# Performance work log

Measured on AMD Instinct MI355X. Metric: run time of the kernel, lower is better.

## Reference

```python
import jax, jax.numpy as jnp
import numpy as np

N = 100000      # num nodes
E = 1600000     # num edges
DIN, H, DOUT = 64, 128, 64
EPS = 1e-5


def setup_inputs() -> dict:
    key = jax.random.key(0)
    ks = jax.random.split(key, 16)
    def w(k, shape):
        fan_in = shape[0]
        return jax.random.normal(k, shape, dtype=jnp.float32) / np.sqrt(fan_in)
    return {
        "x": jax.random.normal(ks[0], (N, DIN), dtype=jnp.float32),
        "edge_index": jax.random.randint(ks[1], (2, E), 0, N, dtype=jnp.int32),
        "W1": w(ks[2], (DIN, H)),  "b1": jnp.zeros((H,), jnp.float32),
        "W2": w(ks[3], (H, H)),    "b2": jnp.zeros((H,), jnp.float32),
        "W3": w(ks[4], (H, DOUT)), "b3": jnp.zeros((DOUT,), jnp.float32),
        "g1": jnp.ones((H,), jnp.float32),  "be1": jnp.zeros((H,), jnp.float32),
        "g2": jnp.ones((H,), jnp.float32),  "be2": jnp.zeros((H,), jnp.float32),
        "Ws1": w(ks[5], (DIN, H)),  "bs1": jnp.zeros((H,), jnp.float32),
        "Ws2": w(ks[6], (H, DOUT)), "bs2": jnp.zeros((DOUT,), jnp.float32),
    }


def _layer_norm(h, g, b):
    m = jnp.mean(h, axis=-1, keepdims=True)
    v = jnp.mean(jnp.square(h - m), axis=-1, keepdims=True)
    return (h - m) * jax.lax.rsqrt(v + EPS) * g + b


def reference(x, edge_index, W1, b1, W2, b2, W3, b3, g1, be1, g2, be2, Ws1, bs1, Ws2, bs2):
    n = x.shape[0]
    # GCNConv: add self-loops, symmetric deg^{-1/2} normalization (PyG default)
    loop = jnp.arange(n, dtype=edge_index.dtype)
    src = jnp.concatenate([edge_index[0], loop])  # [E+N]
    dst = jnp.concatenate([edge_index[1], loop])
    deg = jax.ops.segment_sum(jnp.ones_like(dst, dtype=x.dtype), dst, num_segments=n)
    dinv = jax.lax.rsqrt(deg)  # deg >= 1 thanks to self-loops
    norm = (dinv[src] * dinv[dst])[:, None]  # [E+N, 1]

    def conv(h, W, b):
        hw = h @ W                                   # [n, dout]
        msg = hw[src] * norm                         # gather + scale
        return jax.ops.segment_sum(msg, dst, num_segments=n) + b

    # layer 1: conv -> LN -> relu -> +skip1(x)   (dropout is eval-mode identity)
    x1 = jax.nn.relu(_layer_norm(conv(x, W1, b1), g1, be1)) + (x @ Ws1 + bs1)
    # layer 2: conv -> LN -> relu -> +x1
    x2 = jax.nn.relu(_layer_norm(conv(x1, W2, b2), g2, be2)) + x1
    # layer 3: conv + skip2(x1)
    x3 = conv(x2, W3, b3) + (x1 @ Ws2 + bs2)
    return x3
```

## Files before the change

kernel.cpp:

```cpp
#include <hip/hip_runtime.h>

#define LN_EPS 1e-5f

typedef unsigned short ushortT;

__device__ __forceinline__ float4 ld4(const float* p) { return *reinterpret_cast<const float4*>(p); }
__device__ __forceinline__ void st4(float* p, float4 v) { *reinterpret_cast<float4*>(p) = v; }
__device__ __forceinline__ float bf2f(unsigned u) { return __uint_as_float(u << 16); }
__device__ __forceinline__ unsigned short f2bf(float f) {
    unsigned u = __float_as_uint(f);
    u += 0x7fffu + ((u >> 16) & 1u);
    return (unsigned short)(u >> 16);
}
__device__ __forceinline__ unsigned pack2(float a, float b) {
    return (unsigned)f2bf(a) | ((unsigned)f2bf(b) << 16);
}


__global__ __launch_bounds__(256) void k_zero_i32(int* __restrict__ p, int n) {
    int i = blockIdx.x * 256 + threadIdx.x;
    if (i < n) p[i] = 0;
}

__global__ __launch_bounds__(256) void k_count(const int* __restrict__ dst, int* __restrict__ counts, int E) {
    int i = blockIdx.x * 256 + threadIdx.x;
    if (i < E) atomicAdd(&counts[dst[i]], 1);
}

__global__ __launch_bounds__(256) void k_dinv(const int* __restrict__ counts, float* __restrict__ dinv, int n) {
    int i = blockIdx.x * 256 + threadIdx.x;
    if (i < n) dinv[i] = rsqrtf((float)(counts[i] + 1));
}

__global__ __launch_bounds__(512) void k_scan1(const int* __restrict__ counts, int* __restrict__ bsum, int n) {
    __shared__ int s[512];
    int idx = blockIdx.x * 512 + threadIdx.x;
    s[threadIdx.x] = (idx < n) ? counts[idx] : 0;
    __syncthreads();
    for (int d = 256; d > 0; d >>= 1) {
        if (threadIdx.x < d) s[threadIdx.x] += s[threadIdx.x + d];
        __syncthreads();
    }
    if (threadIdx.x == 0) bsum[blockIdx.x] = s[0];
}

__global__ __launch_bounds__(512) void k_scan2(int* __restrict__ bsum, int nb) {
    __shared__ int s[512];
    int t = threadIdx.x;
    int v = (t < nb) ? bsum[t] : 0;
    s[t] = v;
    __syncthreads();
    for (int d = 1; d < 512; d <<= 1) {
        int tv = (t >= d) ? s[t - d] : 0;
        __syncthreads();
        s[t] += tv;
        __syncthreads();
    }
    if (t < nb) bsum[t] = s[t] - v;
}

__global__ __launch_bounds__(512) void k_scan3(const int* __restrict__ counts, const int* __restrict__ bsum,
                                               int* __restrict__ offsets, int* __restrict__ cursor, int n) {
    __shared__ int s[512];
    int tid = threadIdx.x;
    int idx = blockIdx.x * 512 + tid;
    int v = (idx < n) ? counts[idx] : 0;
    s[tid] = v;
    __syncthreads();
    for (int d = 1; d < 512; d <<= 1) {
        int t = (tid >= d) ? s[tid - d] : 0;
        __syncthreads();
        s[tid] += t;
        __syncthreads();
    }
    if (idx < n) {
        int ex = s[tid] - v + bsum[blockIdx.x];
        offsets[idx] = ex;
        cursor[idx] = ex;
    }
}

__global__ __launch_bounds__(256) void k_fill(const int* __restrict__ src, const int* __restrict__ dst,
                                              const float* __restrict__ dinv, int* __restrict__ cursor,
                                              uint2* __restrict__ csr, int E) {
    int i = blockIdx.x * 256 + threadIdx.x;
    if (i < E) {
        int d = dst[i], s = src[i];
        int p = atomicAdd(&cursor[d], 1);
        uint2 v;
        v.x = (unsigned)s;
        v.y = __float_as_uint(dinv[s]);
        csr[p] = v;
    }
}


__global__ __launch_bounds__(256) void k_cvt_bf16(const float* __restrict__ in, ushortT* __restrict__ o, int n4) {
    int i = blockIdx.x * 256 + threadIdx.x;
    if (i < n4) {
        float4 v = ld4(in + (size_t)i * 4);
        uint2 pk;
        pk.x = pack2(v.x, v.y);
        pk.y = pack2(v.z, v.w);
        *reinterpret_cast<uint2*>(o + (size_t)i * 4) = pk;
    }
}


template <int K, int MINW>
__global__ __launch_bounds__(512, MINW) void k_agg_gemm_ln(
        const ushortT* __restrict__ t16, const uint2* __restrict__ csr,
        const int* __restrict__ rs, const int* __restrict__ re,
        const float* __restrict__ dinv,
        const float* __restrict__ W, const float* __restrict__ bias,
        const float* __restrict__ g, const float* __restrict__ be,
        const float* __restrict__ skip,
        float* __restrict__ out32, ushortT* __restrict__ out16, int n) {
    constexpr int M = 128;
    constexpr int G = K / 8;
    constexpr int NODES = 512 / G;
    constexpr int RPT = NODES / 16;
    constexpr int KH = 32;
    constexpr int KP = K + 8;

    __shared__ float Wl[KH][M];
    __shared__ float Xl[NODES][KP];

    const int tid = threadIdx.x;

    {
        const int grp = tid / G;
        const int sub = tid % G;
        const int node = blockIdx.x * NODES + grp;
        float a[8];
#pragma unroll
        for (int i = 0; i < 8; ++i) a[i] = 0.f;

        if (node < n) {
            const float di = dinv[node];
            const ushortT* base = t16 + sub * 8;
            const int p0 = rs[node], p1 = re[node];

            auto acc8 = [&](uint4 v, float w) {
                a[0] = fmaf(bf2f(v.x & 0xffffu), w, a[0]); a[1] = fmaf(bf2f(v.x >> 16), w, a[1]);
                a[2] = fmaf(bf2f(v.y & 0xffffu), w, a[2]); a[3] = fmaf(bf2f(v.y >> 16), w, a[3]);
                a[4] = fmaf(bf2f(v.z & 0xffffu), w, a[4]); a[5] = fmaf(bf2f(v.z >> 16), w, a[5]);
                a[6] = fmaf(bf2f(v.w & 0xffffu), w, a[6]); a[7] = fmaf(bf2f(v.w >> 16), w, a[7]);
            };

            int p = p0;
            for (; p + 4 <= p1; p += 4) {
                uint2 e0 = csr[p], e1 = csr[p + 1], e2 = csr[p + 2], e3 = csr[p + 3];
                uint4 v0 = *reinterpret_cast<const uint4*>(base + (size_t)e0.x * K);
                uint4 v1 = *reinterpret_cast<const uint4*>(base + (size_t)e1.x * K);
                uint4 v2 = *reinterpret_cast<const uint4*>(base + (size_t)e2.x * K);
                uint4 v3 = *reinterpret_cast<const uint4*>(base + (size_t)e3.x * K);
                acc8(v0, __uint_as_float(e0.y) * di);
                acc8(v1, __uint_as_float(e1.y) * di);
                acc8(v2, __uint_as_float(e2.y) * di);
                acc8(v3, __uint_as_float(e3.y) * di);
            }
            for (; p < p1; ++p) {
                uint2 e0 = csr[p];
                uint4 v0 = *reinterpret_cast<const uint4*>(base + (size_t)e0.x * K);
                acc8(v0, __uint_as_float(e0.y) * di);
            }
            {
                uint4 v = *reinterpret_cast<const uint4*>(base + (size_t)node * K);
                acc8(v, di * di);
            }
        }
        st4(&Xl[grp][sub * 8], make_float4(a[0], a[1], a[2], a[3]));
        st4(&Xl[grp][sub * 8 + 4], make_float4(a[4], a[5], a[6], a[7]));
    }

    const int cg = tid & 31;
    const int rg = tid >> 5;
    const float4 bias4 = ld4(bias + cg * 4);

    float4 acc[RPT];
#pragma unroll
    for (int r = 0; r < RPT; ++r) acc[r] = bias4;

    for (int kh = 0; kh < K; kh += KH) {
        __syncthreads();
        for (int i = tid; i < KH * M / 4; i += 512) {
            int kk = i / (M / 4), c = i % (M / 4);
            st4(&Wl[kk][c * 4], ld4(W + (size_t)(kh + kk) * M + c * 4));
        }
        __syncthreads();
#pragma unroll 4
        for (int kk = 0; kk < KH; ++kk) {
            float4 w4 = ld4(&Wl[kk][cg * 4]);
#pragma unroll
            for (int r = 0; r < RPT; ++r) {
                float xv = Xl[rg * RPT + r][kh + kk];
                acc[r].x = fmaf(xv, w4.x, acc[r].x);
                acc[r].y = fmaf(xv, w4.y, acc[r].y);
                acc[r].z = fmaf(xv, w4.z, acc[r].z);
                acc[r].w = fmaf(xv, w4.w, acc[r].w);
            }
        }
    }

    const float4 g4 = ld4(g + cg * 4);
    const float4 be4 = ld4(be + cg * 4);
#pragma unroll
    for (int r = 0; r < RPT; ++r) {
        int gr = blockIdx.x * NODES + rg * RPT + r;
        if (gr >= n) continue;
        float4 a = acc[r];
        float sum = a.x + a.y + a.z + a.w;
#pragma unroll
        for (int m = 16; m > 0; m >>= 1) sum += __shfl_xor(sum, m, 32);
        const float mean = sum * (1.f / 128.f);
        float dx = a.x - mean, dy = a.y - mean, dz = a.z - mean, dw = a.w - mean;
        float sq = dx * dx + dy * dy + dz * dz + dw * dw;
#pragma unroll
        for (int m = 16; m > 0; m >>= 1) sq += __shfl_xor(sq, m, 32);
        const float rstd = rsqrtf(sq * (1.f / 128.f) + LN_EPS);
        float4 s4 = ld4(skip + (size_t)gr * 128 + cg * 4);
        float4 y;
        y.x = fmaxf(fmaf(dx * rstd, g4.x, be4.x), 0.f) + s4.x;
        y.y = fmaxf(fmaf(dy * rstd, g4.y, be4.y), 0.f) + s4.y;
        y.z = fmaxf(fmaf(dz * rstd, g4.z, be4.z), 0.f) + s4.z;
        y.w = fmaxf(fmaf(dw * rstd, g4.w, be4.w), 0.f) + s4.w;
        st4(out32 + (size_t)gr * 128 + cg * 4, y);
        if (out16) {
            uint2 pk;
            pk.x = pack2(y.x, y.y);
            pk.y = pack2(y.z, y.w);
            *reinterpret_cast<uint2*>(out16 + (size_t)gr * 128 + cg * 4) = pk;
        }
    }
}


__global__ __launch_bounds__(256) void k_final(const ushortT* __restrict__ t16,
                                               const int* __restrict__ rs, const int* __restrict__ re,
                                               const uint2* __restrict__ csr,
                                               const float* __restrict__ dinv, const float* __restrict__ bias,
                                               float* __restrict__ out, int n) {
    constexpr int C = 64, G = 8, NPB = 32;
    const int grp = threadIdx.x / G;
    const int sub = threadIdx.x % G;
    const int node = blockIdx.x * NPB + grp;
    if (node >= n) return;
    const float di = dinv[node];
    float a[8];
#pragma unroll
    for (int i = 0; i < 8; ++i) a[i] = 0.f;
    const ushortT* base = t16 + sub * 8;
    const int p0 = rs[node], p1 = re[node];

    auto acc8 = [&](uint4 v, float w) {
        a[0] = fmaf(bf2f(v.x & 0xffffu), w, a[0]); a[1] = fmaf(bf2f(v.x >> 16), w, a[1]);
        a[2] = fmaf(bf2f(v.y & 0xffffu), w, a[2]); a[3] = fmaf(bf2f(v.y >> 16), w, a[3]);
        a[4] = fmaf(bf2f(v.z & 0xffffu), w, a[4]); a[5] = fmaf(bf2f(v.z >> 16), w, a[5]);
        a[6] = fmaf(bf2f(v.w & 0xffffu), w, a[6]); a[7] = fmaf(bf2f(v.w >> 16), w, a[7]);
    };

    int p = p0;
    for (; p + 4 <= p1; p += 4) {
        uint2 e0 = csr[p], e1 = csr[p + 1], e2 = csr[p + 2], e3 = csr[p + 3];
        uint4 v0 = *reinterpret_cast<const uint4*>(base + (size_t)e0.x * C);
        uint4 v1 = *reinterpret_cast<const uint4*>(base + (size_t)e1.x * C);
        uint4 v2 = *reinterpret_cast<const uint4*>(base + (size_t)e2.x * C);
        uint4 v3 = *reinterpret_cast<const uint4*>(base + (size_t)e3.x * C);
        acc8(v0, __uint_as_float(e0.y) * di);
        acc8(v1, __uint_as_float(e1.y) * di);
        acc8(v2, __uint_as_float(e2.y) * di);
        acc8(v3, __uint_as_float(e3.y) * di);
    }
    for (; p < p1; ++p) {
        uint2 e0 = csr[p];
        uint4 v0 = *reinterpret_cast<const uint4*>(base + (size_t)e0.x * C);
        acc8(v0, __uint_as_float(e0.y) * di);
    }
    {
        uint4 v = *reinterpret_cast<const uint4*>(base + (size_t)node * C);
        acc8(v, di * di);
    }
    float* o = out + (size_t)node * 64 + sub * 8;
    const float* b = bias + sub * 8;
    float4 c0 = ld4(o), c1 = ld4(o + 4);
    float4 b0 = ld4(b), b1 = ld4(b + 4);
    st4(o, make_float4(c0.x + a[0] + b0.x, c0.y + a[1] + b0.y,
                       c0.z + a[2] + b0.z, c0.w + a[3] + b0.w));
    st4(o + 4, make_float4(c1.x + a[4] + b1.x, c1.y + a[5] + b1.y,
                           c1.z + a[6] + b1.z, c1.w + a[7] + b1.w));
}


template <int K, int M, bool BF16OUT>
__global__ __launch_bounds__(256) void gemm_small(const float* __restrict__ in, const float* __restrict__ W,
                                                  const float* __restrict__ bias, void* __restrict__ outp,
                                                  int nrows) {
    constexpr int CG = M / 4;
    constexpr int RG = 256 / CG;
    constexpr int RPT = (M == 128) ? 4 : 2;
    constexpr int ROWS = RG * RPT;
    constexpr int KH = 32;
    constexpr int KP = K + 4;

    __shared__ float Wl[KH][M];
    __shared__ float Xl[ROWS][KP];

    const int tid = threadIdx.x;
    const int cg = tid % CG;
    const int rg = tid / CG;

    float4 bias4 = make_float4(0.f, 0.f, 0.f, 0.f);
    if (bias) bias4 = ld4(bias + cg * 4);

    for (int base = blockIdx.x * ROWS; base < nrows; base += gridDim.x * ROWS) {
        __syncthreads();
        constexpr int NV = ROWS * K / 4;
        for (int i = tid; i < NV; i += 256) {
            int r = i / (K / 4), c = i % (K / 4);
            int gr = base + r;
            float4 v = make_float4(0.f, 0.f, 0.f, 0.f);
            if (gr < nrows) v = ld4(in + (size_t)gr * K + c * 4);
            st4(&Xl[r][c * 4], v);
        }

        float4 acc[RPT];
#pragma unroll
        for (int r = 0; r < RPT; ++r) acc[r] = bias4;

        for (int kh = 0; kh < K; kh += KH) {
            __syncthreads();
            constexpr int WV = KH * M / 4;
            for (int i = tid; i < WV; i += 256) {
                int kk = i / (M / 4), c = i % (M / 4);
                st4(&Wl[kk][c * 4], ld4(W + (size_t)(kh + kk) * M + c * 4));
            }
            __syncthreads();
#pragma unroll 4
            for (int kk = 0; kk < KH; ++kk) {
                float4 w4 = ld4(&Wl[kk][cg * 4]);
#pragma unroll
                for (int r = 0; r < RPT; ++r) {
                    float xv = Xl[rg * RPT + r][kh + kk];
                    acc[r].x = fmaf(xv, w4.x, acc[r].x);
                    acc[r].y = fmaf(xv, w4.y, acc[r].y);
                    acc[r].z = fmaf(xv, w4.z, acc[r].z);
                    acc[r].w = fmaf(xv, w4.w, acc[r].w);
                }
            }
        }
#pragma unroll
        for (int r = 0; r < RPT; ++r) {
            int gr = base + rg * RPT + r;
            if (gr < nrows) {
                if (BF16OUT) {
                    uint2 pk;
                    pk.x = pack2(acc[r].x, acc[r].y);
                    pk.y = pack2(acc[r].z, acc[r].w);
                    *reinterpret_cast<uint2*>((ushortT*)outp + (size_t)gr * M + cg * 4) = pk;
                } else {
                    st4((float*)outp + (size_t)gr * M + cg * 4, acc[r]);
                }
            }
        }
    }
}


extern "C" void kernel_launch(void* const* d_in, const int* in_sizes, int n_in,
                              void* d_out, int out_size, void* d_ws, size_t ws_size,
                              hipStream_t stream) {
    const float* x   = (const float*)d_in[0];
    const int* eidx  = (const int*)d_in[1];
    const float* W1  = (const float*)d_in[2];
    const float* b1  = (const float*)d_in[3];
    const float* W2  = (const float*)d_in[4];
    const float* b2  = (const float*)d_in[5];
    const float* W3  = (const float*)d_in[6];
    const float* b3  = (const float*)d_in[7];
    const float* g1  = (const float*)d_in[8];
    const float* be1 = (const float*)d_in[9];
    const float* g2  = (const float*)d_in[10];
    const float* be2 = (const float*)d_in[11];
    const float* Ws1 = (const float*)d_in[12];
    const float* bs1 = (const float*)d_in[13];
    const float* Ws2 = (const float*)d_in[14];
    const float* bs2 = (const float*)d_in[15];
    float* out = (float*)d_out;

    const int N = in_sizes[0] / 64;
    const int E = in_sizes[1] / 2;
    const int* esrc = eidx;
    const int* edst = eidx + E;

    char* p = (char*)d_ws;
    auto alloc = [&](size_t bytes) -> char* {
        char* q = p;
        p += (bytes + 255) & ~(size_t)255;
        return q;
    };
    float* S      = (float*)alloc((size_t)N * 128 * 4);
    float* X2     = S;
    float* X1     = (float*)alloc((size_t)N * 128 * 4);
    ushortT* x16  = (ushortT*)alloc((size_t)N * 64 * 2);
    ushortT* X1_16  = (ushortT*)alloc((size_t)N * 128 * 2);
    ushortT* HW3_16 = (ushortT*)alloc((size_t)N * 64 * 2);
    uint2* csr    = (uint2*)alloc((size_t)E * 8);
    int* counts   = (int*)alloc((size_t)N * 4);
    int* offsets  = (int*)alloc((size_t)N * 4);
    int* cursor   = (int*)alloc((size_t)N * 4);
    float* dinv   = (float*)alloc((size_t)N * 4);
    const int NB = (N + 511) / 512;
    int* bsum     = (int*)alloc((size_t)NB * 4);

    const int gN256 = (N + 255) / 256;
    const int gE256 = (E + 255) / 256;

    k_zero_i32<<<gN256, 256, 0, stream>>>(counts, N);
    k_count<<<gE256, 256, 0, stream>>>(edst, counts, E);
    k_dinv<<<gN256, 256, 0, stream>>>(counts, dinv, N);
    k_scan1<<<NB, 512, 0, stream>>>(counts, bsum, N);
    k_scan2<<<1, 512, 0, stream>>>(bsum, NB);
    k_scan3<<<NB, 512, 0, stream>>>(counts, bsum, offsets, cursor, N);
    k_fill<<<gE256, 256, 0, stream>>>(esrc, edst, dinv, cursor, csr, E);

    k_cvt_bf16<<<(N * 16 + 255) / 256, 256, 0, stream>>>(x, x16, N * 16);
    gemm_small<64, 128, false><<<(N + 31) / 32, 256, 0, stream>>>(x, Ws1, bs1, S, N);
    k_agg_gemm_ln<64, 6><<<(N + 63) / 64, 512, 0, stream>>>(x16, csr, offsets, cursor, dinv,
                                                            W1, b1, g1, be1, S,
                                                            X1, X1_16, N);

    k_agg_gemm_ln<128, 8><<<(N + 31) / 32, 512, 0, stream>>>(X1_16, csr, offsets, cursor, dinv,
                                                             W2, b2, g2, be2, X1,
                                                             X2, (ushortT*)nullptr, N);

    gemm_small<128, 64, false><<<(N + 31) / 32, 256, 0, stream>>>(X1, Ws2, bs2, out, N);
    gemm_small<128, 64, true><<<(N + 31) / 32, 256, 0, stream>>>(X2, W3, nullptr, HW3_16, N);
    k_final<<<(N + 31) / 32, 256, 0, stream>>>(HW3_16, offsets, cursor, csr,
                                               dinv, b3, out, N);
}
```

Measured before the change: 557.3 us.

## Fuse skip GEMMs into aggregation kernels and shrink CSR to source indices

Folds the layer-1 skip GEMM (x@Ws1) into the layer-1 aggregation kernel, reusing the node's own bf16 row staged in shared memory. Likewise folds the x1@Ws2 skip GEMM and the final aggregation into one layer-3 kernel. The CSR entries drop from 8 to 4 bytes by storing only the source index and looking up dinv[src] during gathering. This removes the fp32 S buffer round trip and two launches, and halves CSR traffic, but adds an extra random dinv gather per edge and computes the skip GEMMs from bf16 inputs instead of fp32, which lowers precision.

```diff
diff --git a/kernel.cpp b/kernel.cpp
--- a/kernel.cpp
+++ b/kernel.cpp
@@ -14,6 +14,13 @@
 }
 __device__ __forceinline__ unsigned pack2(float a, float b) {
     return (unsigned)f2bf(a) | ((unsigned)f2bf(b) << 16);
+}
+
+__device__ __forceinline__ void acc8(float (&a)[8], uint4 v, float wt) {
+    a[0] = fmaf(bf2f(v.x & 0xffffu), wt, a[0]); a[1] = fmaf(bf2f(v.x >> 16), wt, a[1]);
+    a[2] = fmaf(bf2f(v.y & 0xffffu), wt, a[2]); a[3] = fmaf(bf2f(v.y >> 16), wt, a[3]);
+    a[4] = fmaf(bf2f(v.z & 0xffffu), wt, a[4]); a[5] = fmaf(bf2f(v.z >> 16), wt, a[5]);
+    a[6] = fmaf(bf2f(v.w & 0xffffu), wt, a[6]); a[7] = fmaf(bf2f(v.w >> 16), wt, a[7]);
 }
 
 
@@ -81,16 +88,12 @@
 }
 
 __global__ __launch_bounds__(256) void k_fill(const int* __restrict__ src, const int* __restrict__ dst,
-                                              const float* __restrict__ dinv, int* __restrict__ cursor,
-                                              uint2* __restrict__ csr, int E) {
+                                              int* __restrict__ cursor, int* __restrict__ csr, int E) {
     int i = blockIdx.x * 256 + threadIdx.x;
     if (i < E) {
-        int d = dst[i], s = src[i];
+        int d = dst[i];
         int p = atomicAdd(&cursor[d], 1);
-        uint2 v;
-        v.x = (unsigned)s;
-        v.y = __float_as_uint(dinv[s]);
-        csr[p] = v;
+        csr[p] = src[i];
     }
 }
 
@@ -107,30 +110,160 @@
 }
 
 
-template <int K, int MINW>
-__global__ __launch_bounds__(512, MINW) void k_agg_gemm_ln(
-        const ushortT* __restrict__ t16, const uint2* __restrict__ csr,
+__global__ __launch_bounds__(512, 8) void k_l1_fused(
+        const ushortT* __restrict__ x16, const int* __restrict__ csr,
+        const int* __restrict__ rs, const int* __restrict__ re,
+        const float* __restrict__ dinv,
+        const float* __restrict__ W1, const float* __restrict__ b1,
+        const float* __restrict__ g1, const float* __restrict__ be1,
+        const float* __restrict__ Ws1, const float* __restrict__ bs1,
+        float* __restrict__ X1, ushortT* __restrict__ X1_16, int n) {
+    constexpr int NODES = 64, G = 8, KP = 72;
+    __shared__ float Xl[NODES][KP];
+    __shared__ ushortT Xown[NODES][KP];
+    __shared__ float Wl[16][128];
+
+    const int tid = threadIdx.x;
+
+    {
+        const int grp = tid / G, sub = tid % G;
+        const int node = blockIdx.x * NODES + grp;
+        float a[8];
+#pragma unroll
+        for (int i = 0; i < 8; ++i) a[i] = 0.f;
+        uint4 own = make_uint4(0u, 0u, 0u, 0u);
+
+        if (node < n) {
+            const float di = dinv[node];
+            const ushortT* base = x16 + sub * 8;
+            const int p0 = rs[node], p1 = re[node];
+            int p = p0;
+            for (; p + 4 <= p1; p += 4) {
+                int s0 = csr[p], s1 = csr[p + 1], s2 = csr[p + 2], s3 = csr[p + 3];
+                float w0 = dinv[s0] * di, w1 = dinv[s1] * di, w2 = dinv[s2] * di, w3 = dinv[s3] * di;
+                uint4 v0 = *reinterpret_cast<const uint4*>(base + (size_t)s0 * 64);
+                uint4 v1 = *reinterpret_cast<const uint4*>(base + (size_t)s1 * 64);
+                uint4 v2 = *reinterpret_cast<const uint4*>(base + (size_t)s2 * 64);
+                uint4 v3 = *reinterpret_cast<const uint4*>(base + (size_t)s3 * 64);
+                acc8(a, v0, w0); acc8(a, v1, w1); acc8(a, v2, w2); acc8(a, v3, w3);
+            }
+            for (; p < p1; ++p) {
+                int s0 = csr[p];
+                float w0 = dinv[s0] * di;
+                uint4 v0 = *reinterpret_cast<const uint4*>(base + (size_t)s0 * 64);
+                acc8(a, v0, w0);
+            }
+            own = *reinterpret_cast<const uint4*>(base + (size_t)node * 64);
+            acc8(a, own, di * di);
+        }
+        st4(&Xl[grp][sub * 8], make_float4(a[0], a[1], a[2], a[3]));
+        st4(&Xl[grp][sub * 8 + 4], make_float4(a[4], a[5], a[6], a[7]));
+        *reinterpret_cast<uint4*>(&Xown[grp][sub * 8]) = own;
+    }
+
+    const int cg = tid & 31;
+    const int rg = tid >> 5;
+    const float4 b1_4 = ld4(b1 + cg * 4);
+    float4 acc[4];
+#pragma unroll
+    for (int r = 0; r < 4; ++r) acc[r] = b1_4;
+
+    for (int kh = 0; kh < 64; kh += 16) {
+        __syncthreads();
+        {
+            int kk = tid >> 5, c = tid & 31;
+            st4(&Wl[kk][c * 4], ld4(W1 + (size_t)(kh + kk) * 128 + c * 4));
+        }
+        __syncthreads();
+#pragma unroll 4
+        for (int kk = 0; kk < 16; ++kk) {
+            float4 w4 = ld4(&Wl[kk][cg * 4]);
+#pragma unroll
+            for (int r = 0; r < 4; ++r) {
+                float xv = Xl[rg * 4 + r][kh + kk];
+                acc[r].x = fmaf(xv, w4.x, acc[r].x);
+                acc[r].y = fmaf(xv, w4.y, acc[r].y);
+                acc[r].z = fmaf(xv, w4.z, acc[r].z);
+                acc[r].w = fmaf(xv, w4.w, acc[r].w);
+            }
+        }
+    }
+
+    const float4 g4 = ld4(g1 + cg * 4);
+    const float4 be4 = ld4(be1 + cg * 4);
+#pragma unroll
+    for (int r = 0; r < 4; ++r) {
+        float4 a = acc[r];
+        float sum = a.x + a.y + a.z + a.w;
+#pragma unroll
+        for (int m = 16; m > 0; m >>= 1) sum += __shfl_xor(sum, m, 32);
+        const float mean = sum * (1.f / 128.f);
+        float dx = a.x - mean, dy = a.y - mean, dz = a.z - mean, dw = a.w - mean;
+        float sq = dx * dx + dy * dy + dz * dz + dw * dw;
+#pragma unroll
+        for (int m = 16; m > 0; m >>= 1) sq += __shfl_xor(sq, m, 32);
+        const float rstd = rsqrtf(sq * (1.f / 128.f) + LN_EPS);
+        acc[r].x = fmaxf(fmaf(dx * rstd, g4.x, be4.x), 0.f);
+        acc[r].y = fmaxf(fmaf(dy * rstd, g4.y, be4.y), 0.f);
+        acc[r].z = fmaxf(fmaf(dz * rstd, g4.z, be4.z), 0.f);
+        acc[r].w = fmaxf(fmaf(dw * rstd, g4.w, be4.w), 0.f);
+    }
+
+    for (int kh = 0; kh < 64; kh += 16) {
+        __syncthreads();
+        {
+            int kk = tid >> 5, c = tid & 31;
+            st4(&Wl[kk][c * 4], ld4(Ws1 + (size_t)(kh + kk) * 128 + c * 4));
+        }
+        __syncthreads();
+#pragma unroll 4
+        for (int kk = 0; kk < 16; kk += 2) {
+            float4 wa = ld4(&Wl[kk][cg * 4]);
+            float4 wb = ld4(&Wl[kk + 1][cg * 4]);
+#pragma unroll
+            for (int r = 0; r < 4; ++r) {
+                unsigned xp = *reinterpret_cast<const unsigned*>(&Xown[rg * 4 + r][kh + kk]);
+                float x0 = bf2f(xp & 0xffffu), x1 = bf2f(xp >> 16);
+                acc[r].x = fmaf(x0, wa.x, acc[r].x); acc[r].y = fmaf(x0, wa.y, acc[r].y);
+                acc[r].z = fmaf(x0, wa.z, acc[r].z); acc[r].w = fmaf(x0, wa.w, acc[r].w);
+                acc[r].x = fmaf(x1, wb.x, acc[r].x); acc[r].y = fmaf(x1, wb.y, acc[r].y);
+                acc[r].z = fmaf(x1, wb.z, acc[r].z); acc[r].w = fmaf(x1, wb.w, acc[r].w);
+            }
+        }
+    }
+
+    const float4 bs4 = ld4(bs1 + cg * 4);
+#pragma unroll
+    for (int r = 0; r < 4; ++r) {
+        int gr = blockIdx.x * NODES + rg * 4 + r;
+        if (gr >= n) continue;
+        float4 y = make_float4(acc[r].x + bs4.x, acc[r].y + bs4.y,
+                               acc[r].z + bs4.z, acc[r].w + bs4.w);
+        st4(X1 + (size_t)gr * 128 + cg * 4, y);
+        uint2 pk;
+        pk.x = pack2(y.x, y.y);
+        pk.y = pack2(y.z, y.w);
+        *reinterpret_cast<uint2*>(X1_16 + (size_t)gr * 128 + cg * 4) = pk;
+    }
+}
+
+
+__global__ __launch_bounds__(512, 8) void k_l2_fused(
+        const ushortT* __restrict__ t16, const int* __restrict__ csr,
         const int* __restrict__ rs, const int* __restrict__ re,
         const float* __restrict__ dinv,
         const float* __restrict__ W, const float* __restrict__ bias,
         const float* __restrict__ g, const float* __restrict__ be,
         const float* __restrict__ skip,
-        float* __restrict__ out32, ushortT* __restrict__ out16, int n) {
-    constexpr int M = 128;
-    constexpr int G = K / 8;
-    constexpr int NODES = 512 / G;
-    constexpr int RPT = NODES / 16;
-    constexpr int KH = 32;
-    constexpr int KP = K + 8;
-
-    __shared__ float Wl[KH][M];
+        float* __restrict__ out32, int n) {
+    constexpr int NODES = 32, G = 16, KP = 136, KH = 32;
+    __shared__ float Wl[KH][128];
     __shared__ float Xl[NODES][KP];
 
     const int tid = threadIdx.x;
 
     {
-        const int grp = tid / G;
-        const int sub = tid % G;
+        const int grp = tid / G, sub = tid % G;
         const int node = blockIdx.x * NODES + grp;
         float a[8];
 #pragma unroll
@@ -140,35 +273,24 @@
             const float di = dinv[node];
             const ushortT* base = t16 + sub * 8;
             const int p0 = rs[node], p1 = re[node];
-
-            auto acc8 = [&](uint4 v, float w) {
-                a[0] = fmaf(bf2f(v.x & 0xffffu), w, a[0]); a[1] = fmaf(bf2f(v.x >> 16), w, a[1]);
-                a[2] = fmaf(bf2f(v.y & 0xffffu), w, a[2]); a[3] = fmaf(bf2f(v.y >> 16), w, a[3]);
-                a[4] = fmaf(bf2f(v.z & 0xffffu), w, a[4]); a[5] = fmaf(bf2f(v.z >> 16), w, a[5]);
-                a[6] = fmaf(bf2f(v.w & 0xffffu), w, a[6]); a[7] = fmaf(bf2f(v.w >> 16), w, a[7]);
-            };
-
             int p = p0;
             for (; p + 4 <= p1; p += 4) {
-                uint2 e0 = csr[p], e1 = csr[p + 1], e2 = csr[p + 2], e3 = csr[p + 3];
-                uint4 v0 = *reinterpret_cast<const uint4*>(base + (size_t)e0.x * K);
-                uint4 v1 = *reinterpret_cast<const uint4*>(base + (size_t)e1.x * K);
-                uint4 v2 = *reinterpret_cast<const uint4*>(base + (size_t)e2.x * K);
-                uint4 v3 = *reinterpret_cast<const uint4*>(base + (size_t)e3.x * K);
-                acc8(v0, __uint_as_float(e0.y) * di);
-                acc8(v1, __uint_as_float(e1.y) * di);
-                acc8(v2, __uint_as_float(e2.y) * di);
-                acc8(v3, __uint_as_float(e3.y) * di);
+                int s0 = csr[p], s1 = csr[p + 1], s2 = csr[p + 2], s3 = csr[p + 3];
+                float w0 = dinv[s0] * di, w1 = dinv[s1] * di, w2 = dinv[s2] * di, w3 = dinv[s3] * di;
+                uint4 v0 = *reinterpret_cast<const uint4*>(base + (size_t)s0 * 128);
+                uint4 v1 = *reinterpret_cast<const uint4*>(base + (size_t)s1 * 128);
+                uint4 v2 = *reinterpret_cast<const uint4*>(base + (size_t)s2 * 128);
+                uint4 v3 = *reinterpret_cast<const uint4*>(base + (size_t)s3 * 128);
+                acc8(a, v0, w0); acc8(a, v1, w1); acc8(a, v2, w2); acc8(a, v3, w3);
             }
             for (; p < p1; ++p) {
-                uint2 e0 = csr[p];
-                uint4 v0 = *reinterpret_cast<const uint4*>(base + (size_t)e0.x * K);
-                acc8(v0, __uint_as_float(e0.y) * di);
-            }
-            {
-                uint4 v = *reinterpret_cast<const uint4*>(base + (size_t)node * K);
-                acc8(v, di * di);
-            }
+                int s0 = csr[p];
+                float w0 = dinv[s0] * di;
+                uint4 v0 = *reinterpret_cast<const uint4*>(base + (size_t)s0 * 128);
+                acc8(a, v0, w0);
+            }
+            uint4 v = *reinterpret_cast<const uint4*>(base + (size_t)node * 128);
+            acc8(a, v, di * di);
         }
         st4(&Xl[grp][sub * 8], make_float4(a[0], a[1], a[2], a[3]));
         st4(&Xl[grp][sub * 8 + 4], make_float4(a[4], a[5], a[6], a[7]));
@@ -177,24 +299,22 @@
     const int cg = tid & 31;
     const int rg = tid >> 5;
     const float4 bias4 = ld4(bias + cg * 4);
-
-    float4 acc[RPT];
-#pragma unroll
-    for (int r = 0; r < RPT; ++r) acc[r] = bias4;
-
-    for (int kh = 0; kh < K; kh += KH) {
-        __syncthreads();
-        for (int i = tid; i < KH * M / 4; i += 512) {
-            int kk = i / (M / 4), c = i % (M / 4);
-            st4(&Wl[kk][c * 4], ld4(W + (size_t)(kh + kk) * M + c * 4));
+    float4 acc[2];
+    acc[0] = bias4; acc[1] = bias4;
+
+    for (int kh = 0; kh < 128; kh += KH) {
+        __syncthreads();
+        for (int i = tid; i < KH * 32; i += 512) {
+            int kk = i >> 5, c = i & 31;
+            st4(&Wl[kk][c * 4], ld4(W + (size_t)(kh + kk) * 128 + c * 4));
         }
         __syncthreads();
 #pragma unroll 4
         for (int kk = 0; kk < KH; ++kk) {
             float4 w4 = ld4(&Wl[kk][cg * 4]);
 #pragma unroll
-            for (int r = 0; r < RPT; ++r) {
-                float xv = Xl[rg * RPT + r][kh + kk];
+            for (int r = 0; r < 2; ++r) {
+                float xv = Xl[rg * 2 + r][kh + kk];
                 acc[r].x = fmaf(xv, w4.x, acc[r].x);
                 acc[r].y = fmaf(xv, w4.y, acc[r].y);
                 acc[r].z = fmaf(xv, w4.z, acc[r].z);
@@ -206,8 +326,8 @@
     const float4 g4 = ld4(g + cg * 4);
     const float4 be4 = ld4(be + cg * 4);
 #pragma unroll
-    for (int r = 0; r < RPT; ++r) {
-        int gr = blockIdx.x * NODES + rg * RPT + r;
+    for (int r = 0; r < 2; ++r) {
+        int gr = blockIdx.x * NODES + rg * 2 + r;
         if (gr >= n) continue;
         float4 a = acc[r];
         float sum = a.x + a.y + a.z + a.w;
@@ -226,82 +346,111 @@
         y.z = fmaxf(fmaf(dz * rstd, g4.z, be4.z), 0.f) + s4.z;
         y.w = fmaxf(fmaf(dw * rstd, g4.w, be4.w), 0.f) + s4.w;
         st4(out32 + (size_t)gr * 128 + cg * 4, y);
-        if (out16) {
-            uint2 pk;
-            pk.x = pack2(y.x, y.y);
-            pk.y = pack2(y.z, y.w);
-            *reinterpret_cast<uint2*>(out16 + (size_t)gr * 128 + cg * 4) = pk;
-        }
-    }
-}
-
-
-__global__ __launch_bounds__(256) void k_final(const ushortT* __restrict__ t16,
-                                               const int* __restrict__ rs, const int* __restrict__ re,
-                                               const uint2* __restrict__ csr,
-                                               const float* __restrict__ dinv, const float* __restrict__ bias,
-                                               float* __restrict__ out, int n) {
-    constexpr int C = 64, G = 8, NPB = 32;
-    const int grp = threadIdx.x / G;
-    const int sub = threadIdx.x % G;
-    const int node = blockIdx.x * NPB + grp;
-    if (node >= n) return;
-    const float di = dinv[node];
-    float a[8];
-#pragma unroll
-    for (int i = 0; i < 8; ++i) a[i] = 0.f;
-    const ushortT* base = t16 + sub * 8;
-    const int p0 = rs[node], p1 = re[node];
-
-    auto acc8 = [&](uint4 v, float w) {
-        a[0] = fmaf(bf2f(v.x & 0xffffu), w, a[0]); a[1] = fmaf(bf2f(v.x >> 16), w, a[1]);
-        a[2] = fmaf(bf2f(v.y & 0xffffu), w, a[2]); a[3] = fmaf(bf2f(v.y >> 16), w, a[3]);
-        a[4] = fmaf(bf2f(v.z & 0xffffu), w, a[4]); a[5] = fmaf(bf2f(v.z >> 16), w, a[5]);
-        a[6] = fmaf(bf2f(v.w & 0xffffu), w, a[6]); a[7] = fmaf(bf2f(v.w >> 16), w, a[7]);
-    };
-
-    int p = p0;
-    for (; p + 4 <= p1; p += 4) {
-        uint2 e0 = csr[p], e1 = csr[p + 1], e2 = csr[p + 2], e3 = csr[p + 3];
-        uint4 v0 = *reinterpret_cast<const uint4*>(base + (size_t)e0.x * C);
-        uint4 v1 = *reinterpret_cast<const uint4*>(base + (size_t)e1.x * C);
-        uint4 v2 = *reinterpret_cast<const uint4*>(base + (size_t)e2.x * C);
-        uint4 v3 = *reinterpret_cast<const uint4*>(base + (size_t)e3.x * C);
-        acc8(v0, __uint_as_float(e0.y) * di);
-        acc8(v1, __uint_as_float(e1.y) * di);
-        acc8(v2, __uint_as_float(e2.y) * di);
-        acc8(v3, __uint_as_float(e3.y) * di);
-    }
-    for (; p < p1; ++p) {
-        uint2 e0 = csr[p];
-        uint4 v0 = *reinterpret_cast<const uint4*>(base + (size_t)e0.x * C);
-        acc8(v0, __uint_as_float(e0.y) * di);
-    }
+    }
+}
+
+
+__global__ __launch_bounds__(512, 8) void k_l3_fused(
+        const ushortT* __restrict__ hw16, const ushortT* __restrict__ x1_16,
+        const int* __restrict__ csr, const int* __restrict__ rs, const int* __restrict__ re,
+        const float* __restrict__ dinv,
+        const float* __restrict__ Ws2, const float* __restrict__ bs2, const float* __restrict__ b3,
+        float* __restrict__ out, int n) {
+    constexpr int NODES = 64, G = 8;
+    __shared__ float Xl[NODES][72];
+    __shared__ ushortT Xown[NODES][136];
+    __shared__ float Wl[16][64];
+
+    const int tid = threadIdx.x;
+
     {
-        uint4 v = *reinterpret_cast<const uint4*>(base + (size_t)node * C);
-        acc8(v, di * di);
-    }
-    float* o = out + (size_t)node * 64 + sub * 8;
-    const float* b = bias + sub * 8;
-    float4 c0 = ld4(o), c1 = ld4(o + 4);
-    float4 b0 = ld4(b), b1 = ld4(b + 4);
-    st4(o, make_float4(c0.x + a[0] + b0.x, c0.y + a[1] + b0.y,
-                       c0.z + a[2] + b0.z, c0.w + a[3] + b0.w));
-    st4(o + 4, make_float4(c1.x + a[4] + b1.x, c1.y + a[5] + b1.y,
-                           c1.z + a[6] + b1.z, c1.w + a[7] + b1.w));
-}
-
-
-template <int K, int M, bool BF16OUT>
-__global__ __launch_bounds__(256) void gemm_small(const float* __restrict__ in, const float* __restrict__ W,
-                                                  const float* __restrict__ bias, void* __restrict__ outp,
-                                                  int nrows) {
-    constexpr int CG = M / 4;
-    constexpr int RG = 256 / CG;
-    constexpr int RPT = (M == 128) ? 4 : 2;
-    constexpr int ROWS = RG * RPT;
-    constexpr int KH = 32;
-    constexpr int KP = K + 4;
+        const int grp = tid / G, sub = tid % G;
+        const int node = blockIdx.x * NODES + grp;
+        float a[8];
+#pragma unroll
+        for (int i = 0; i < 8; ++i) a[i] = 0.f;
+        uint4 o0 = make_uint4(0u, 0u, 0u, 0u), o1 = o0;
+
+        if (node < n) {
+            const float di = dinv[node];
+            const ushortT* base = hw16 + sub * 8;
+            const int p0 = rs[node], p1 = re[node];
+            int p = p0;
+            for (; p + 4 <= p1; p += 4) {
+                int s0 = csr[p], s1 = csr[p + 1], s2 = csr[p + 2], s3 = csr[p + 3];
+                float w0 = dinv[s0] * di, w1 = dinv[s1] * di, w2 = dinv[s2] * di, w3 = dinv[s3] * di;
+                uint4 v0 = *reinterpret_cast<const uint4*>(base + (size_t)s0 * 64);
+                uint4 v1 = *reinterpret_cast<const uint4*>(base + (size_t)s1 * 64);
+                uint4 v2 = *reinterpret_cast<const uint4*>(base + (size_t)s2 * 64);
+                uint4 v3 = *reinterpret_cast<const uint4*>(base + (size_t)s3 * 64);
+                acc8(a, v0, w0); acc8(a, v1, w1); acc8(a, v2, w2); acc8(a, v3, w3);
+            }
+            for (; p < p1; ++p) {
+                int s0 = csr[p];
+                float w0 = dinv[s0] * di;
+                uint4 v0 = *reinterpret_cast<const uint4*>(base + (size_t)s0 * 64);
+                acc8(a, v0, w0);
+            }
+            uint4 v = *reinterpret_cast<const uint4*>(base + (size_t)node * 64);
+            acc8(a, v, di * di);
+            const uint4* xr = reinterpret_cast<const uint4*>(x1_16 + (size_t)node * 128 + sub * 16);
+            o0 = xr[0];
+            o1 = xr[1];
+        }
+        st4(&Xl[grp][sub * 8], make_float4(a[0], a[1], a[2], a[3]));
+        st4(&Xl[grp][sub * 8 + 4], make_float4(a[4], a[5], a[6], a[7]));
+        *reinterpret_cast<uint4*>(&Xown[grp][sub * 16]) = o0;
+        *reinterpret_cast<uint4*>(&Xown[grp][sub * 16 + 8]) = o1;
+    }
+
+    __syncthreads();
+
+    const int cg = tid & 15;
+    const int rg = tid >> 4;
+    const float4 b3_4 = ld4(b3 + cg * 4);
+    const float4 bs2_4 = ld4(bs2 + cg * 4);
+    float4 acc[2];
+#pragma unroll
+    for (int r = 0; r < 2; ++r) {
+        float4 ag = ld4(&Xl[rg * 2 + r][cg * 4]);
+        acc[r] = make_float4(ag.x + b3_4.x + bs2_4.x, ag.y + b3_4.y + bs2_4.y,
+                             ag.z + b3_4.z + bs2_4.z, ag.w + b3_4.w + bs2_4.w);
+    }
+
+    for (int kh = 0; kh < 128; kh += 16) {
+        __syncthreads();
+        if (tid < 256) {
+            int kk = tid >> 4, c = tid & 15;
+            st4(&Wl[kk][c * 4], ld4(Ws2 + (size_t)(kh + kk) * 64 + c * 4));
+        }
+        __syncthreads();
+#pragma unroll 4
+        for (int kk = 0; kk < 16; kk += 2) {
+            float4 wa = ld4(&Wl[kk][cg * 4]);
+            float4 wb = ld4(&Wl[kk + 1][cg * 4]);
+#pragma unroll
+            for (int r = 0; r < 2; ++r) {
+                unsigned xp = *reinterpret_cast<const unsigned*>(&Xown[rg * 2 + r][kh + kk]);
+                float x0 = bf2f(xp & 0xffffu), x1 = bf2f(xp >> 16);
+                acc[r].x = fmaf(x0, wa.x, acc[r].x); acc[r].y = fmaf(x0, wa.y, acc[r].y);
+                acc[r].z = fmaf(x0, wa.z, acc[r].z); acc[r].w = fmaf(x0, wa.w, acc[r].w);
+                acc[r].x = fmaf(x1, wb.x, acc[r].x); acc[r].y = fmaf(x1, wb.y, acc[r].y);
+                acc[r].z = fmaf(x1, wb.z, acc[r].z); acc[r].w = fmaf(x1, wb.w, acc[r].w);
+            }
+        }
+    }
+
+#pragma unroll
+    for (int r = 0; r < 2; ++r) {
+        int gr = blockIdx.x * NODES + rg * 2 + r;
+        if (gr < n) st4(out + (size_t)gr * 64 + cg * 4, acc[r]);
+    }
+}
+
+
+__global__ __launch_bounds__(256) void gemm_hw3(const float* __restrict__ in, const float* __restrict__ W,
+                                                ushortT* __restrict__ outp, int nrows) {
+    constexpr int K = 128, M = 64, CG = 16, RPT = 2, ROWS = 32, KH = 32, KP = K + 4;
 
     __shared__ float Wl[KH][M];
     __shared__ float Xl[ROWS][KP];
@@ -310,13 +459,9 @@
     const int cg = tid % CG;
     const int rg = tid / CG;
 
-    float4 bias4 = make_float4(0.f, 0.f, 0.f, 0.f);
-    if (bias) bias4 = ld4(bias + cg * 4);
-
     for (int base = blockIdx.x * ROWS; base < nrows; base += gridDim.x * ROWS) {
         __syncthreads();
-        constexpr int NV = ROWS * K / 4;
-        for (int i = tid; i < NV; i += 256) {
+        for (int i = tid; i < ROWS * K / 4; i += 256) {
             int r = i / (K / 4), c = i % (K / 4);
             int gr = base + r;
             float4 v = make_float4(0.f, 0.f, 0.f, 0.f);
@@ -326,12 +471,11 @@
 
         float4 acc[RPT];
 #pragma unroll
-        for (int r = 0; r < RPT; ++r) acc[r] = bias4;
+        for (int r = 0; r < RPT; ++r) acc[r] = make_float4(0.f, 0.f, 0.f, 0.f);
 
         for (int kh = 0; kh < K; kh += KH) {
             __syncthreads();
-            constexpr int WV = KH * M / 4;
-            for (int i = tid; i < WV; i += 256) {
+            for (int i = tid; i < KH * M / 4; i += 256) {
                 int kk = i / (M / 4), c = i % (M / 4);
                 st4(&Wl[kk][c * 4], ld4(W + (size_t)(kh + kk) * M + c * 4));
             }
@@ -353,14 +497,10 @@
         for (int r = 0; r < RPT; ++r) {
             int gr = base + rg * RPT + r;
             if (gr < nrows) {
-                if (BF16OUT) {
-                    uint2 pk;
-                    pk.x = pack2(acc[r].x, acc[r].y);
-                    pk.y = pack2(acc[r].z, acc[r].w);
-                    *reinterpret_cast<uint2*>((ushortT*)outp + (size_t)gr * M + cg * 4) = pk;
-                } else {
-                    st4((float*)outp + (size_t)gr * M + cg * 4, acc[r]);
-                }
+                uint2 pk;
+                pk.x = pack2(acc[r].x, acc[r].y);
+                pk.y = pack2(acc[r].z, acc[r].w);
+                *reinterpret_cast<uint2*>(outp + (size_t)gr * M + cg * 4) = pk;
             }
         }
     }
@@ -399,19 +539,18 @@
         p += (bytes + 255) & ~(size_t)255;
         return q;
     };
-    float* S      = (float*)alloc((size_t)N * 128 * 4);
-    float* X2     = S;
-    float* X1     = (float*)alloc((size_t)N * 128 * 4);
-    ushortT* x16  = (ushortT*)alloc((size_t)N * 64 * 2);
+    float* X1       = (float*)alloc((size_t)N * 128 * 4);
+    float* X2       = (float*)alloc((size_t)N * 128 * 4);
+    ushortT* x16    = (ushortT*)alloc((size_t)N * 64 * 2);
     ushortT* X1_16  = (ushortT*)alloc((size_t)N * 128 * 2);
     ushortT* HW3_16 = (ushortT*)alloc((size_t)N * 64 * 2);
-    uint2* csr    = (uint2*)alloc((size_t)E * 8);
-    int* counts   = (int*)alloc((size_t)N * 4);
-    int* offsets  = (int*)alloc((size_t)N * 4);
-    int* cursor   = (int*)alloc((size_t)N * 4);
-    float* dinv   = (float*)alloc((size_t)N * 4);
+    int* csr        = (int*)alloc((size_t)E * 4);
+    int* counts     = (int*)alloc((size_t)N * 4);
+    int* offsets    = (int*)alloc((size_t)N * 4);
+    int* cursor     = (int*)alloc((size_t)N * 4);
+    float* dinv     = (float*)alloc((size_t)N * 4);
     const int NB = (N + 511) / 512;
-    int* bsum     = (int*)alloc((size_t)NB * 4);
+    int* bsum       = (int*)alloc((size_t)NB * 4);
 
     const int gN256 = (N + 255) / 256;
     const int gE256 = (E + 255) / 256;
@@ -422,20 +561,17 @@
     k_scan1<<<NB, 512, 0, stream>>>(counts, bsum, N);
     k_scan2<<<1, 512, 0, stream>>>(bsum, NB);
     k_scan3<<<NB, 512, 0, stream>>>(counts, bsum, offsets, cursor, N);
-    k_fill<<<gE256, 256, 0, stream>>>(esrc, edst, dinv, cursor, csr, E);
+    k_fill<<<gE256, 256, 0, stream>>>(esrc, edst, cursor, csr, E);
 
     k_cvt_bf16<<<(N * 16 + 255) / 256, 256, 0, stream>>>(x, x16, N * 16);
-    gemm_small<64, 128, false><<<(N + 31) / 32, 256, 0, stream>>>(x, Ws1, bs1, S, N);
-    k_agg_gemm_ln<64, 6><<<(N + 63) / 64, 512, 0, stream>>>(x16, csr, offsets, cursor, dinv,
-                                                            W1, b1, g1, be1, S,
-                                                            X1, X1_16, N);
-
-    k_agg_gemm_ln<128, 8><<<(N + 31) / 32, 512, 0, stream>>>(X1_16, csr, offsets, cursor, dinv,
-                                                             W2, b2, g2, be2, X1,
-                                                             X2, (ushortT*)nullptr, N);
-
-    gemm_small<128, 64, false><<<(N + 31) / 32, 256, 0, stream>>>(X1, Ws2, bs2, out, N);
-    gemm_small<128, 64, true><<<(N + 31) / 32, 256, 0, stream>>>(X2, W3, nullptr, HW3_16, N);
-    k_final<<<(N + 31) / 32, 256, 0, stream>>>(HW3_16, offsets, cursor, csr,
-                                               dinv, b3, out, N);
-}
+    k_l1_fused<<<(N + 63) / 64, 512, 0, stream>>>(x16, csr, offsets, cursor, dinv,
+                                                  W1, b1, g1, be1, Ws1, bs1,
+                                                  X1, X1_16, N);
+
+    k_l2_fused<<<(N + 31) / 32, 512, 0, stream>>>(X1_16, csr, offsets, cursor, dinv,
+                                                  W2, b2, g2, be2, X1, X2, N);
+
+    gemm_hw3<<<(N + 31) / 32, 256, 0, stream>>>(X2, W3, HW3_16, N);
+    k_l3_fused<<<(N + 63) / 64, 512, 0, stream>>>(HW3_16, X1_16, csr, offsets, cursor,
+                                                  dinv, Ws2, bs2, b3, out, N);
+}
```

Result: no change. 567.4 us (+1.8%).
